# Optimization experiments

Hardware: AMD Instinct MI355X
Metric: run time of the kernel (lower is better)

Reference implementation:

```python
import jax, jax.numpy as jnp
import numpy as np
import math

B, S, D, H = 1, 4096, 1024, 16
DH = D // H


def setup_inputs() -> dict:
    key = jax.random.key(0)
    k1, k2, k3 = jax.random.split(key, 3)
    x = jax.random.normal(k1, (B, S, D), dtype=jnp.float32)
    # additive causal mask: 0 where allowed, -1e9 where masked (future)
    causal = jnp.tril(jnp.ones((S, S), dtype=bool))
    mask = jnp.where(causal, 0.0, -1e9).astype(jnp.float32)[None]  # [1,S,S]
    W_attn = jax.random.normal(k2, (D, 3 * D), dtype=jnp.float32) * 0.02
    b_attn = jnp.zeros((3 * D,), dtype=jnp.float32)
    W_proj = jax.random.normal(k3, (D, D), dtype=jnp.float32) * 0.02
    b_proj = jnp.zeros((D,), dtype=jnp.float32)
    return {"x": x, "mask": mask, "W_attn": W_attn, "b_attn": b_attn,
            "W_proj": W_proj, "b_proj": b_proj}


def reference(x, mask, W_attn, b_attn, W_proj, b_proj):
    # c_attn: fused QKV projection
    qkv = x @ W_attn + b_attn                      # [B,S,3D]
    q, k, v = jnp.split(qkv, 3, axis=-1)           # each [B,S,D]

    def heads(t):  # [B,S,D] -> [B,H,S,DH]
        return t.reshape(B, S, H, DH).transpose(0, 2, 1, 3)

    q, k, v = heads(q), heads(k), heads(v)
    # scores: eager O(S^2) matrix as in original
    w = jnp.einsum('bhqd,bhkd->bhqk', q, k) / math.sqrt(DH)
    w = w + mask[:, None, :, :]                    # broadcast over heads
    w = jax.nn.softmax(w, axis=-1)                 # dropout p=0 -> identity
    a = jnp.einsum('bhqk,bhkd->bhqd', w, v)        # [B,H,S,DH]
    a = a.transpose(0, 2, 1, 3).reshape(B, S, D)   # merge heads
    return a @ W_proj + b_proj
```

## Files before the change

kernel.cpp:

```cpp
#include <hip/hip_runtime.h>

typedef _Float16 half8 __attribute__((ext_vector_type(8)));
typedef short short8 __attribute__((ext_vector_type(8)));
typedef float floatx4 __attribute__((ext_vector_type(4)));

static __device__ __forceinline__ float bf2f(unsigned short u) {
  union { unsigned int u; float f; } c; c.u = ((unsigned int)u) << 16; return c.f;
}
static __device__ __forceinline__ unsigned short f2bf(float f) {
  union { float f; unsigned int u; } c; c.f = f;
  return (unsigned short)((c.u + 0x7fffu + ((c.u >> 16) & 1u)) >> 16);
}
static __device__ __forceinline__ unsigned short f2h(float f) {
  union { _Float16 h; unsigned short u; } c; c.h = (_Float16)f; return c.u;
}
static __device__ __forceinline__ unsigned int cvtpk(float a, float b) {
  unsigned int r;
  asm("v_cvt_pk_bf16_f32 %0, %1, %2" : "=v"(r) : "v"(a), "v"(b));
  return r;
}

#define GL2LDS16(gsrc, ldst)                                                        \
  __builtin_amdgcn_global_load_lds(                                                 \
      (const __attribute__((address_space(1))) void*)(const void*)(gsrc),           \
      (__attribute__((address_space(3))) void*)(void*)(ldst), 16, 0, 0)

static __device__ __forceinline__ int dtype_bf16(const unsigned short* mask16) {
  return mask16[1] != 0;
}

__global__ __launch_bounds__(256) void k_prep(const void* __restrict__ x,
    const void* __restrict__ Wa, const void* __restrict__ Wp,
    const unsigned short* __restrict__ mask16, _Float16* __restrict__ xh,
    _Float16* __restrict__ WaT, _Float16* __restrict__ WpT) {
  __shared__ float tile[64 * 65];
  const int dt = dtype_bf16(mask16);
  const int bx = blockIdx.x;
  const int tid = threadIdx.x;
  if (bx < 4096) {
    const int i = (bx * 256 + tid) * 4;
    _Float16 o[4];
    if (dt) {
      ushort4 u = *((const ushort4*)((const unsigned short*)x + i));
      o[0] = (_Float16)bf2f(u.x); o[1] = (_Float16)bf2f(u.y);
      o[2] = (_Float16)bf2f(u.z); o[3] = (_Float16)bf2f(u.w);
    } else {
      float4 f = *((const float4*)((const float*)x + i));
      o[0] = (_Float16)f.x; o[1] = (_Float16)f.y;
      o[2] = (_Float16)f.z; o[3] = (_Float16)f.w;
    }
    union { _Float16 h[4]; uint2 u; } pk;
    pk.h[0] = o[0]; pk.h[1] = o[1]; pk.h[2] = o[2]; pk.h[3] = o[3];
    *((uint2*)(xh + i)) = pk.u;
    return;
  }
  const void* in; _Float16* out; int n0, k0, N;
  if (bx < 4864) { const int b = bx - 4096; in = Wa; out = WaT; N = 3072;
                   n0 = (b % 48) * 64; k0 = (b / 48) * 64; }
  else           { const int b = bx - 4864; in = Wp; out = WpT; N = 1024;
                   n0 = (b % 16) * 64; k0 = (b / 16) * 64; }
  const int r = tid >> 2;
#pragma unroll
  for (int it = 0; it < 4; ++it) {
    const int c4 = (tid & 3) + it * 4;
    const size_t src = (size_t)(k0 + r) * N + n0 + c4 * 4;
    float v[4];
    if (dt) {
      ushort4 u = *((const ushort4*)((const unsigned short*)in + src));
      v[0] = bf2f(u.x); v[1] = bf2f(u.y); v[2] = bf2f(u.z); v[3] = bf2f(u.w);
    } else {
      float4 f = *((const float4*)((const float*)in + src));
      v[0] = f.x; v[1] = f.y; v[2] = f.z; v[3] = f.w;
    }
#pragma unroll
    for (int jj = 0; jj < 4; ++jj) tile[r * 65 + c4 * 4 + jj] = v[jj];
  }
  __syncthreads();
#pragma unroll
  for (int it = 0; it < 4; ++it) {
    const int rn = (tid >> 4) + it * 16;
    const int kc = tid & 15;
    union { _Float16 h[4]; uint2 u; } pk;
#pragma unroll
    for (int jj = 0; jj < 4; ++jj)
      pk.h[jj] = (_Float16)tile[(kc * 4 + jj) * 65 + rn];
    *(uint2*)(out + (size_t)(n0 + rn) * 1024 + k0 + kc * 4) = pk.u;
  }
}

template <int KD>
static __device__ __forceinline__ void gemm_mainloop(const _Float16* __restrict__ A,
    const _Float16* __restrict__ Bt, int m0, int n0,
    _Float16* As, _Float16* Bs, floatx4 acc[4][4]) {
  const int tid = threadIdx.x;
  const int wave = tid >> 6, lane = tid & 63;
  const int lq = lane & 15, quad = lane >> 4;
  const int wm = (wave >> 1) * 64, wn = (wave & 1) * 64;
  const int scol = (lane & 3) * 8;
  for (int k0 = 0; k0 < KD; k0 += 32) {
    __syncthreads();
#pragma unroll
    for (int op = 0; op < 2; ++op) {
      const int rbase = wave * 32 + op * 16;
      const int row = rbase + (lane >> 2);
      GL2LDS16(A + (size_t)(m0 + row) * KD + k0 + scol, As + rbase * 32);
      GL2LDS16(Bt + (size_t)(n0 + row) * KD + k0 + scol, Bs + rbase * 32);
    }
    __builtin_amdgcn_s_waitcnt(0x0f70);
    __syncthreads();
    half8 af[4], bf[4];
#pragma unroll
    for (int i = 0; i < 4; ++i) {
      af[i] = *(const half8*)(As + (wm + i * 16 + lq) * 32 + quad * 8);
      bf[i] = *(const half8*)(Bs + (wn + i * 16 + lq) * 32 + quad * 8);
    }
#pragma unroll
    for (int i = 0; i < 4; ++i)
#pragma unroll
      for (int j = 0; j < 4; ++j)
        acc[i][j] = __builtin_amdgcn_mfma_f32_16x16x32_f16(af[i], bf[j], acc[i][j], 0, 0, 0);
  }
}

__global__ __launch_bounds__(256, 1) void k_gemm_qkv(const _Float16* __restrict__ A,
    const _Float16* __restrict__ Bt, const void* __restrict__ bias,
    const unsigned short* __restrict__ mask16, _Float16* __restrict__ Qb,
    _Float16* __restrict__ Kb, unsigned short* __restrict__ VTb) {
  __shared__ __attribute__((aligned(16))) unsigned short smem[128 * 136];
  _Float16* As = (_Float16*)smem;
  _Float16* Bs = As + 4096;
  const int tid = threadIdx.x, wave = tid >> 6, lane = tid & 63;
  const int lq = lane & 15, quad = lane >> 4;
  const int m0 = blockIdx.y * 128, n0 = blockIdx.x * 128;
  const int wm = (wave >> 1) * 64, wn = (wave & 1) * 64;
  floatx4 acc[4][4] = {};
  gemm_mainloop<1024>(A, Bt, m0, n0, As, Bs, acc);
  const int dt = dtype_bf16(mask16);
  const int sec = n0 >> 10;
  const float scale = (sec == 0) ? 0.1803368801f : 1.0f;
  __syncthreads();
#pragma unroll
  for (int i = 0; i < 4; ++i) {
    const int lmb = wm + i * 16 + quad * 4;
#pragma unroll
    for (int j = 0; j < 4; ++j) {
      const int ln = wn + j * 16 + lq;
      const int gcol = n0 + ln;
      const float bv = dt ? bf2f(((const unsigned short*)bias)[gcol])
                          : ((const float*)bias)[gcol];
#pragma unroll
      for (int r = 0; r < 4; ++r) {
        const float v = (acc[i][j][r] + bv) * scale;
        const unsigned short bits = (sec == 2) ? f2bf(v) : f2h(v);
        if (sec == 2) smem[ln * 136 + lmb + r] = bits;
        else          smem[(lmb + r) * 136 + ln] = bits;
      }
    }
  }
  __syncthreads();
  if (sec == 2) {
#pragma unroll
    for (int it = 0; it < 8; ++it) {
      const int row = (tid >> 4) + it * 16;
      const int ch = tid & 15;
      const uint4 v = *(const uint4*)&smem[row * 136 + ch * 8];
      *(uint4*)(VTb + (size_t)(n0 + row - 2048) * 4096 + m0 + ch * 8) = v;
    }
  } else {
    _Float16* dst = (sec == 0) ? Qb : Kb;
#pragma unroll
    for (int it = 0; it < 8; ++it) {
      const int row = (tid >> 4) + it * 16;
      const int ch = tid & 15;
      const uint4 v = *(const uint4*)&smem[row * 136 + ch * 8];
      const int c = (n0 & 1023) + ch * 8;
      const int hh = c >> 6, dh = c & 63;
      *(uint4*)(dst + ((size_t)(hh * 4096 + m0 + row)) * 64 + dh) = v;
    }
  }
}

__global__ __launch_bounds__(256, 2) void k_attn(const _Float16* __restrict__ Qb,
    const _Float16* __restrict__ Kb, const unsigned short* __restrict__ VTb,
    unsigned short* __restrict__ Op0, unsigned short* __restrict__ Op1,
    unsigned short* __restrict__ Op2, unsigned short* __restrict__ Op3,
    float* __restrict__ Lp) {
  constexpr int S = 4096;
  const int bx = blockIdx.x;
  const int h  = bx & 15;
  const int pr = (bx >> 4) & 7;
  const int cj = bx >> 7;
  const int kbg = 15 - pr;
  const int ksm = pr;
  const int sB  = 64 - 4 * pr;
  const int fb  = sB / 17;
  const int p0 = cj * 17, p1 = p0 + 17;
  const int tid = threadIdx.x, wave = tid >> 6, lane = tid & 63;
  const int lq = lane & 15, quad = lane >> 4;
  __shared__ __attribute__((aligned(16))) _Float16 Ks[64 * 72];
  __shared__ __attribute__((aligned(16))) unsigned short VTs[64 * 72];
  const _Float16* Qh = Qb + (size_t)h * S * 64;
  const _Float16* Kh = Kb + (size_t)h * S * 64;
  const unsigned short* VTh = VTb + (size_t)h * 64 * S;
  short8 aones;
#pragma unroll
  for (int jj = 0; jj < 8; ++jj) aones[jj] = (short)0x3F80;
  const int srow = tid >> 2, schunk = (tid & 3) * 16;

#define LOADQ()                                                                     \
  {                                                                                 \
    const int qb0 = 256 * ku + wave * 64;                                           \
    _Pragma("unroll")                                                               \
    for (int m = 0; m < 4; ++m)                                                     \
      _Pragma("unroll")                                                             \
      for (int ch = 0; ch < 2; ++ch)                                                \
        qf[m][ch] = *(const half8*)(Qh + (size_t)(qb0 + m * 16 + lq) * 64           \
                                    + ch * 32 + quad * 8);                          \
  }
#define ZEROACC()                                                                   \
  {                                                                                 \
    _Pragma("unroll")                                                               \
    for (int nf = 0; nf < 4; ++nf)                                                  \
      _Pragma("unroll")                                                             \
      for (int m = 0; m < 4; ++m) o[nf][m] = (floatx4){0.f, 0.f, 0.f, 0.f};         \
    _Pragma("unroll")                                                               \
    for (int m = 0; m < 4; ++m) ol[m] = (floatx4){0.f, 0.f, 0.f, 0.f};              \
  }
#define EPILOGUE(SLOT)                                                              \
  {                                                                                 \
    const int sl = (SLOT);                                                          \
    unsigned short* Ob = sl == 0 ? Op0 : sl == 1 ? Op1 : sl == 2 ? Op2 : Op3;       \
    const int r0 = sl << 10;                                                        \
    const int qb0 = 256 * ku + wave * 64;                                           \
    _Pragma("unroll")                                                               \
    for (int m = 0; m < 4; ++m) {                                                   \
      const int q = qb0 + m * 16 + lq;                                              \
      _Pragma("unroll")                                                             \
      for (int nf = 0; nf < 4; ++nf) {                                              \
        union { unsigned short u[4]; uint2 v; } pk;                                 \
        _Pragma("unroll")                                                           \
        for (int r = 0; r < 4; ++r) pk.u[r] = f2bf(o[nf][m][r]);                    \
        *(uint2*)(Ob + (size_t)(q - r0) * 1024 + h * 64 + nf * 16 + quad * 4) =     \
            pk.v;                                                                   \
      }                                                                             \
      if (quad == 0) Lp[sl * 65536 + h * 4096 + q] = ol[m][0];                      \
    }                                                                               \
  }

  int ku = (p0 < sB) ? kbg : ksm;
  half8 qf[4][2];
  floatx4 o[4][4];
  floatx4 ol[4];
  LOADQ();
  ZEROACC();
  uint4 kreg0, kreg1, vreg0, vreg1;
  {
    const int t0 = (p0 < sB) ? p0 : p0 - sB;
    const int kt = t0 * 64;
    kreg0 = *(const uint4*)(Kh + (size_t)(kt + srow) * 64 + schunk);
    kreg1 = *(const uint4*)(Kh + (size_t)(kt + srow) * 64 + schunk + 8);
    vreg0 = *(const uint4*)(VTh + (size_t)srow * S + kt + schunk);
    vreg1 = *(const uint4*)(VTh + (size_t)srow * S + kt + schunk + 8);
  }
  for (int pos = p0; pos < p1; ++pos) {
    if (pos == sB) {
      EPILOGUE(cj);
      ku = ksm;
      LOADQ();
      ZEROACC();
    }
    const int t = (pos < sB) ? pos : pos - sB;
    const int kt = t * 64;
    __syncthreads();
    *(uint4*)(Ks + srow * 72 + schunk) = kreg0;
    *(uint4*)(Ks + srow * 72 + schunk + 8) = kreg1;
    *(uint4*)(VTs + srow * 72 + schunk) = vreg0;
    *(uint4*)(VTs + srow * 72 + schunk + 8) = vreg1;
    __syncthreads();
    if (pos + 1 < p1) {
      const int nx = pos + 1;
      const int tn = (nx < sB) ? nx : nx - sB;
      const int kn = tn * 64;
      kreg0 = *(const uint4*)(Kh + (size_t)(kn + srow) * 64 + schunk);
      kreg1 = *(const uint4*)(Kh + (size_t)(kn + srow) * 64 + schunk + 8);
      vreg0 = *(const uint4*)(VTh + (size_t)srow * S + kn + schunk);
      vreg1 = *(const uint4*)(VTh + (size_t)srow * S + kn + schunk + 8);
    }
    const int qb0 = 256 * ku + wave * 64;
    if ((wave >= 2) || (t < 4 * ku + 2)) {
#pragma unroll
      for (int c = 0; c < 2; ++c) {
        floatx4 sc[4][2];
        {
          half8 kf0[2], kf1[2];
#pragma unroll
          for (int kb = 0; kb < 2; ++kb) {
            const int row = (c * 2 + kb) * 16 + lq;
            kf0[kb] = *(const half8*)(Ks + row * 72 + quad * 8);
            kf1[kb] = *(const half8*)(Ks + row * 72 + 32 + quad * 8);
          }
          __builtin_amdgcn_s_setprio(1);
#pragma unroll
          for (int m = 0; m < 4; ++m)
#pragma unroll
            for (int kb = 0; kb < 2; ++kb) {
              floatx4 z = {0.f, 0.f, 0.f, 0.f};
              z = __builtin_amdgcn_mfma_f32_16x16x32_f16(kf0[kb], qf[m][0], z, 0, 0, 0);
              sc[m][kb] = __builtin_amdgcn_mfma_f32_16x16x32_f16(kf1[kb], qf[m][1], z, 0, 0, 0);
            }
          __builtin_amdgcn_s_setprio(0);
        }
        short8 pf[4];
#pragma unroll
        for (int m = 0; m < 4; ++m) {
          unsigned int dw0, dw1, dw2, dw3;
          if (kt + c * 32 + 31 > qb0 + m * 16) {
            const int q = qb0 + m * 16 + lq;
            float pv0[4], pv1[4];
#pragma unroll
            for (int r = 0; r < 4; ++r) {
              const int key0 = kt + (c * 2 + 0) * 16 + quad * 4 + r;
              const int key1 = kt + (c * 2 + 1) * 16 + quad * 4 + r;
              const float e0 = __builtin_amdgcn_exp2f(sc[m][0][r]);
              const float e1 = __builtin_amdgcn_exp2f(sc[m][1][r]);
              pv0[r] = (key0 > q) ? 0.f : e0;
              pv1[r] = (key1 > q) ? 0.f : e1;
            }
            dw0 = cvtpk(pv0[0], pv0[1]); dw1 = cvtpk(pv0[2], pv0[3]);
            dw2 = cvtpk(pv1[0], pv1[1]); dw3 = cvtpk(pv1[2], pv1[3]);
          } else {
            float pv0[4], pv1[4];
#pragma unroll
            for (int r = 0; r < 4; ++r) {
              pv0[r] = __builtin_amdgcn_exp2f(sc[m][0][r]);
              pv1[r] = __builtin_amdgcn_exp2f(sc[m][1][r]);
            }
            dw0 = cvtpk(pv0[0], pv0[1]); dw1 = cvtpk(pv0[2], pv0[3]);
            dw2 = cvtpk(pv1[0], pv1[1]); dw3 = cvtpk(pv1[2], pv1[3]);
          }
          asm("v_permlane32_swap_b32 %0, %1" : "+v"(dw0), "+v"(dw2));
          asm("v_permlane32_swap_b32 %0, %1" : "+v"(dw1), "+v"(dw3));
          asm("v_permlane16_swap_b32 %0, %1" : "+v"(dw0), "+v"(dw2));
          asm("v_permlane16_swap_b32 %0, %1" : "+v"(dw1), "+v"(dw3));
          union { unsigned int d[4]; short8 s; } u;
          u.d[0] = dw0; u.d[1] = dw1; u.d[2] = dw2; u.d[3] = dw3;
          pf[m] = u.s;
        }
        __builtin_amdgcn_s_setprio(1);
#pragma unroll
        for (int nf = 0; nf < 4; ++nf) {
          const short8 vfr = *(const short8*)(VTs + (nf * 16 + lq) * 72 + c * 32 + quad * 8);
#pragma unroll
          for (int m = 0; m < 4; ++m)
            o[nf][m] = __builtin_amdgcn_mfma_f32_16x16x32_bf16(vfr, pf[m], o[nf][m], 0, 0, 0);
        }
#pragma unroll
        for (int m = 0; m < 4; ++m)
          ol[m] = __builtin_amdgcn_mfma_f32_16x16x32_bf16(aones, pf[m], ol[m], 0, 0, 0);
        __builtin_amdgcn_s_setprio(0);
      }
    }
  }
  EPILOGUE((p1 <= sB) ? cj : cj - fb);
#undef LOADQ
#undef ZEROACC
#undef EPILOGUE
}

__global__ __launch_bounds__(256) void k_merge(const unsigned short* __restrict__ Op0,
    const unsigned short* __restrict__ Op1, const unsigned short* __restrict__ Op2,
    const unsigned short* __restrict__ Op3, const float* __restrict__ Lp,
    _Float16* __restrict__ Ah) {
  const int row = blockIdx.x;
  const int c = threadIdx.x * 4;
  const int h = c >> 6;
  const int k = row >> 8;
  const int n = (k >= 8) ? (4 * k + 20) / 17 : 4 - (64 - 4 * k) / 17;
  float l = 0.f, v0 = 0.f, v1 = 0.f, v2 = 0.f, v3 = 0.f;
#pragma unroll
  for (int s = 0; s < 4; ++s) {
    if (s < n) {
      const unsigned short* Ob = s == 0 ? Op0 : s == 1 ? Op1 : s == 2 ? Op2 : Op3;
      l += Lp[s * 65536 + h * 4096 + row];
      const ushort4 a = *(const ushort4*)(Ob + (size_t)(row - (s << 10)) * 1024 + c);
      v0 += bf2f(a.x); v1 += bf2f(a.y); v2 += bf2f(a.z); v3 += bf2f(a.w);
    }
  }
  const float inv = __builtin_amdgcn_rcpf(l);
  union { _Float16 h4[4]; uint2 u; } pk;
  pk.h4[0] = (_Float16)(v0 * inv);
  pk.h4[1] = (_Float16)(v1 * inv);
  pk.h4[2] = (_Float16)(v2 * inv);
  pk.h4[3] = (_Float16)(v3 * inv);
  *(uint2*)(Ah + (size_t)row * 1024 + c) = pk.u;
}

__global__ __launch_bounds__(256, 1) void k_gemm_proj(const _Float16* __restrict__ A,
    const _Float16* __restrict__ Bt, const void* __restrict__ bias,
    const unsigned short* __restrict__ mask16, void* __restrict__ out) {
  __shared__ __attribute__((aligned(16))) _Float16 As[64 * 32];
  __shared__ __attribute__((aligned(16))) _Float16 Bs[128 * 32];
  __shared__ __attribute__((aligned(16))) float Cs[64 * 132];
  const int tid = threadIdx.x, wave = tid >> 6, lane = tid & 63;
  const int lq = lane & 15, quad = lane >> 4;
  const int m0 = blockIdx.y * 64, n0 = blockIdx.x * 128;
  const int wm = (wave >> 1) * 32, wn = (wave & 1) * 64;
  const int scol = (lane & 3) * 8;
  floatx4 acc[2][4] = {};
  for (int k0 = 0; k0 < 1024; k0 += 32) {
    __syncthreads();
    {
      const int arow = wave * 16 + (lane >> 2);
      GL2LDS16(A + (size_t)(m0 + arow) * 1024 + k0 + scol, As + wave * 16 * 32);
#pragma unroll
      for (int op = 0; op < 2; ++op) {
        const int rbase = wave * 32 + op * 16;
        const int row = rbase + (lane >> 2);
        GL2LDS16(Bt + (size_t)(n0 + row) * 1024 + k0 + scol, Bs + rbase * 32);
      }
    }
    __builtin_amdgcn_s_waitcnt(0x0f70);
    __syncthreads();
    half8 af[2], bf[4];
#pragma unroll
    for (int i = 0; i < 2; ++i)
      af[i] = *(const half8*)(As + (wm + i * 16 + lq) * 32 + quad * 8);
#pragma unroll
    for (int j = 0; j < 4; ++j)
      bf[j] = *(const half8*)(Bs + (wn + j * 16 + lq) * 32 + quad * 8);
#pragma unroll
    for (int i = 0; i < 2; ++i)
#pragma unroll
      for (int j = 0; j < 4; ++j)
        acc[i][j] = __builtin_amdgcn_mfma_f32_16x16x32_f16(af[i], bf[j], acc[i][j], 0, 0, 0);
  }
  const int dt = dtype_bf16(mask16);
#pragma unroll
  for (int i = 0; i < 2; ++i) {
    const int lrow = wm + i * 16 + quad * 4;
#pragma unroll
    for (int j = 0; j < 4; ++j) {
      const int lcol = wn + j * 16 + lq;
      const float bv = dt ? bf2f(((const unsigned short*)bias)[n0 + lcol])
                          : ((const float*)bias)[n0 + lcol];
#pragma unroll
      for (int r = 0; r < 4; ++r)
        Cs[(lrow + r) * 132 + lcol] = acc[i][j][r] + bv;
    }
  }
  __syncthreads();
  if (dt) {
#pragma unroll
    for (int it = 0; it < 8; ++it) {
      const int row = (tid >> 5) + it * 8;
      const int ch = (tid & 31) * 4;
      union { unsigned short u[4]; uint2 v; } pk;
#pragma unroll
      for (int jj = 0; jj < 4; ++jj) pk.u[jj] = f2bf(Cs[row * 132 + ch + jj]);
      *(uint2*)((unsigned short*)out + (size_t)(m0 + row) * 1024 + n0 + ch) = pk.v;
    }
  } else {
#pragma unroll
    for (int it = 0; it < 8; ++it) {
      const int row = (tid >> 5) + it * 8;
      const int ch = (tid & 31) * 4;
      float4 v;
      v.x = Cs[row * 132 + ch + 0];
      v.y = Cs[row * 132 + ch + 1];
      v.z = Cs[row * 132 + ch + 2];
      v.w = Cs[row * 132 + ch + 3];
      *(float4*)((float*)out + (size_t)(m0 + row) * 1024 + n0 + ch) = v;
    }
  }
}

extern "C" void kernel_launch(void* const* d_in, const int* in_sizes, int n_in,
                              void* d_out, int out_size, void* d_ws, size_t ws_size,
                              hipStream_t stream) {
  const void* x    = d_in[0];
  const unsigned short* mask16 = (const unsigned short*)d_in[1];
  const void* Wa   = d_in[2];
  const void* ba   = d_in[3];
  const void* Wp   = d_in[4];
  const void* bp   = d_in[5];
  char* ws = (char*)d_ws;
  _Float16* WpT       = (_Float16*)(ws + 0);
  _Float16* WaT       = (_Float16*)(ws + 2097152);
  float*    Lp        = (float*)   (ws + 2097152);
  unsigned short* Op2 = (unsigned short*)(ws + 3145728);
  _Float16* xh        = (_Float16*)(ws + 8388608);
  unsigned short* Op0 = (unsigned short*)(ws + 8388608);
  _Float16* Qb        = (_Float16*)(ws + 16777216);
  _Float16* Ah        = (_Float16*)(ws + 16777216);
  _Float16* Kb        = (_Float16*)(ws + 25165824);
  unsigned short* VTb = (unsigned short*)(ws + 33554432);
  unsigned short* Op1 = (unsigned short*)(ws + 41943040);
  unsigned short* Op3 = (unsigned short*)(ws + 48234496);

  k_prep<<<5120, 256, 0, stream>>>(x, Wa, Wp, mask16, xh, WaT, WpT);
  { dim3 g(24, 32); k_gemm_qkv<<<g, 256, 0, stream>>>(xh, WaT, ba, mask16, Qb, Kb, VTb); }
  k_attn<<<512, 256, 0, stream>>>(Qb, Kb, VTb, Op0, Op1, Op2, Op3, Lp);
  k_merge<<<4096, 256, 0, stream>>>(Op0, Op1, Op2, Op3, Lp, Ah);
  { dim3 g(8, 64);  k_gemm_proj<<<g, 256, 0, stream>>>(Ah, WpT, bp, mask16, d_out); }
}
```

Baseline: 237.7 us.

## Double-buffer K/V tiles in LDS to drop one barrier per iteration

```diff
diff --git a/kernel.cpp b/kernel.cpp
--- a/kernel.cpp
+++ b/kernel.cpp
@@ -197,8 +197,8 @@
   const int p0 = cj * 17, p1 = p0 + 17;
   const int tid = threadIdx.x, wave = tid >> 6, lane = tid & 63;
   const int lq = lane & 15, quad = lane >> 4;
-  __shared__ __attribute__((aligned(16))) _Float16 Ks[64 * 72];
-  __shared__ __attribute__((aligned(16))) unsigned short VTs[64 * 72];
+  __shared__ __attribute__((aligned(16))) _Float16 Ks[2 * 64 * 72];
+  __shared__ __attribute__((aligned(16))) unsigned short VTs[2 * 64 * 72];
   const _Float16* Qh = Qb + (size_t)h * S * 64;
   const _Float16* Kh = Kb + (size_t)h * S * 64;
   const unsigned short* VTh = VTb + (size_t)h * 64 * S;
@@ -246,6 +246,15 @@
       if (quad == 0) Lp[sl * 65536 + h * 4096 + q] = ol[m][0];                      \
     }                                                                               \
   }
+#define PREFETCH(POS)                                                               \
+  {                                                                                 \
+    const int tn = ((POS) < sB) ? (POS) : (POS)-sB;                                 \
+    const int kn = tn * 64;                                                         \
+    kreg0 = *(const uint4*)(Kh + (size_t)(kn + srow) * 64 + schunk);                \
+    kreg1 = *(const uint4*)(Kh + (size_t)(kn + srow) * 64 + schunk + 8);            \
+    vreg0 = *(const uint4*)(VTh + (size_t)srow * S + kn + schunk);                  \
+    vreg1 = *(const uint4*)(VTh + (size_t)srow * S + kn + schunk + 8);              \
+  }
 
   int ku = (p0 < sB) ? kbg : ksm;
   half8 qf[4][2];
@@ -254,38 +263,34 @@
   LOADQ();
   ZEROACC();
   uint4 kreg0, kreg1, vreg0, vreg1;
-  {
-    const int t0 = (p0 < sB) ? p0 : p0 - sB;
-    const int kt = t0 * 64;
-    kreg0 = *(const uint4*)(Kh + (size_t)(kt + srow) * 64 + schunk);
-    kreg1 = *(const uint4*)(Kh + (size_t)(kt + srow) * 64 + schunk + 8);
-    vreg0 = *(const uint4*)(VTh + (size_t)srow * S + kt + schunk);
-    vreg1 = *(const uint4*)(VTh + (size_t)srow * S + kt + schunk + 8);
-  }
+  PREFETCH(p0);
+  *(uint4*)(Ks + srow * 72 + schunk) = kreg0;
+  *(uint4*)(Ks + srow * 72 + schunk + 8) = kreg1;
+  *(uint4*)(VTs + srow * 72 + schunk) = vreg0;
+  *(uint4*)(VTs + srow * 72 + schunk + 8) = vreg1;
+  if (p0 + 1 < p1) PREFETCH(p0 + 1);
+  __syncthreads();
   for (int pos = p0; pos < p1; ++pos) {
+    const int b = (pos - p0) & 1;
     if (pos == sB) {
       EPILOGUE(cj);
       ku = ksm;
       LOADQ();
       ZEROACC();
     }
+    const _Float16* KsR = Ks + b * 4608;
+    const unsigned short* VsR = VTs + b * 4608;
+    if (pos + 1 < p1) {
+      _Float16* KsW = Ks + (b ^ 1) * 4608;
+      unsigned short* VsW = VTs + (b ^ 1) * 4608;
+      *(uint4*)(KsW + srow * 72 + schunk) = kreg0;
+      *(uint4*)(KsW + srow * 72 + schunk + 8) = kreg1;
+      *(uint4*)(VsW + srow * 72 + schunk) = vreg0;
+      *(uint4*)(VsW + srow * 72 + schunk + 8) = vreg1;
+      if (pos + 2 < p1) PREFETCH(pos + 2);
+    }
     const int t = (pos < sB) ? pos : pos - sB;
     const int kt = t * 64;
-    __syncthreads();
-    *(uint4*)(Ks + srow * 72 + schunk) = kreg0;
-    *(uint4*)(Ks + srow * 72 + schunk + 8) = kreg1;
-    *(uint4*)(VTs + srow * 72 + schunk) = vreg0;
-    *(uint4*)(VTs + srow * 72 + schunk + 8) = vreg1;
-    __syncthreads();
-    if (pos + 1 < p1) {
-      const int nx = pos + 1;
-      const int tn = (nx < sB) ? nx : nx - sB;
-      const int kn = tn * 64;
-      kreg0 = *(const uint4*)(Kh + (size_t)(kn + srow) * 64 + schunk);
-      kreg1 = *(const uint4*)(Kh + (size_t)(kn + srow) * 64 + schunk + 8);
-      vreg0 = *(const uint4*)(VTh + (size_t)srow * S + kn + schunk);
-      vreg1 = *(const uint4*)(VTh + (size_t)srow * S + kn + schunk + 8);
-    }
     const int qb0 = 256 * ku + wave * 64;
     if ((wave >= 2) || (t < 4 * ku + 2)) {
 #pragma unroll
@@ -296,8 +301,8 @@
 #pragma unroll
           for (int kb = 0; kb < 2; ++kb) {
             const int row = (c * 2 + kb) * 16 + lq;
-            kf0[kb] = *(const half8*)(Ks + row * 72 + quad * 8);
-            kf1[kb] = *(const half8*)(Ks + row * 72 + 32 + quad * 8);
+            kf0[kb] = *(const half8*)(KsR + row * 72 + quad * 8);
+            kf1[kb] = *(const half8*)(KsR + row * 72 + 32 + quad * 8);
           }
           __builtin_amdgcn_s_setprio(1);
 #pragma unroll
@@ -349,7 +354,7 @@
         __builtin_amdgcn_s_setprio(1);
 #pragma unroll
         for (int nf = 0; nf < 4; ++nf) {
-          const short8 vfr = *(const short8*)(VTs + (nf * 16 + lq) * 72 + c * 32 + quad * 8);
+          const short8 vfr = *(const short8*)(VsR + (nf * 16 + lq) * 72 + c * 32 + quad * 8);
 #pragma unroll
           for (int m = 0; m < 4; ++m)
             o[nf][m] = __builtin_amdgcn_mfma_f32_16x16x32_bf16(vfr, pf[m], o[nf][m], 0, 0, 0);
@@ -360,11 +365,13 @@
         __builtin_amdgcn_s_setprio(0);
       }
     }
+    __syncthreads();
   }
   EPILOGUE((p1 <= sB) ? cj : cj - fb);
 #undef LOADQ
 #undef ZEROACC
 #undef EPILOGUE
+#undef PREFETCH
 }
 
 __global__ __launch_bounds__(256) void k_merge(const unsigned short* __restrict__ Op0,
```

After: 242.0 us. About the same (+1.8%).
